# Kernel tuning notes

Hardware: AMD Instinct MI355X
Metric: run time of the kernel (lower is better)

The kernel has to match this reference:

```python
import jax, jax.numpy as jnp
import numpy as np

LN_EPS = 1e-5

def sin_emb(coords, dim):
    # coords [..., 3] -> [..., dim]; dim split evenly over 3 axes, sin/cos halves
    per_axis = dim // 3
    half = per_axis // 2
    freqs = jnp.exp(-jnp.log(10000.0) * jnp.arange(half, dtype=coords.dtype) / max(half - 1, 1))
    ang = coords[..., None] * freqs  # [..., 3, half]
    emb = jnp.concatenate([jnp.sin(ang), jnp.cos(ang)], axis=-1)  # [..., 3, per_axis]
    return emb.reshape(coords.shape[:-1] + (dim,))

def layernorm(x, g, b):
    mu = jnp.mean(x, axis=-1, keepdims=True)
    var = jnp.mean((x - mu) ** 2, axis=-1, keepdims=True)
    return (x - mu) * jax.lax.rsqrt(var + LN_EPS) * g + b

def point_mlp(x, w, b, g, be, act):
    h = layernorm(x @ w + b, g, be)
    return jax.nn.gelu(h, approximate=False) if act else h

def query_ball_point(radius, nsample, xyz):
    # xyz [B,N,3] -> idx [B,N,nsample] (pad with first in-ball index, PointNet++ style)
    N = xyz.shape[1]
    sq = jnp.sum((xyz[:, :, None, :] - xyz[:, None, :, :]) ** 2, axis=-1)  # [B,N,N]
    idx0 = jnp.where(sq > radius * radius, N, jnp.arange(N)[None, None, :])
    idx = jnp.sort(idx0, axis=-1)[:, :, :nsample]
    return jnp.where(idx == N, idx[:, :, :1], idx)

def index_points(points, idx):
    # points [B,N,C], idx [B,S,K] -> [B,S,K,C]
    return jax.vmap(lambda p, i: p[i])(points, idx)

def setup_inputs() -> dict:
    key = jax.random.key(0)
    ks = jax.random.split(key, 20)
    B, N, C_stem, C_tok = 4, 4096, 64, 256
    C_in = C_stem + 3 + 24 + 96  # 187
    w = lambda k, i, o: jax.random.normal(k, (i, o), jnp.float32) * 0.02
    inp = {
        'xyz': jax.random.uniform(ks[0], (B, N, 3), jnp.float32),
        'point_feature': jax.random.normal(ks[1], (B, N, C_stem), jnp.float32),
        # scene_point_mlp
        'w1': w(ks[2], C_in, C_tok), 'b1': jnp.zeros((C_tok,)), 'g1': jnp.ones((C_tok,)), 'be1': jnp.zeros((C_tok,)),
        'w2': w(ks[3], C_tok, C_tok), 'b2': jnp.zeros((C_tok,)), 'g2': jnp.ones((C_tok,)), 'be2': jnp.zeros((C_tok,)),
        # scene_projection
        'pw1': w(ks[4], C_tok, C_tok), 'pb1': jnp.zeros((C_tok,)), 'pg1': jnp.ones((C_tok,)), 'pbe1': jnp.zeros((C_tok,)),
        'pw2': w(ks[5], C_tok, C_tok), 'pb2': jnp.zeros((C_tok,)), 'pg2': jnp.ones((C_tok,)), 'pbe2': jnp.zeros((C_tok,)),
    }
    return inp

def reference(xyz, point_feature, w1, b1, g1, be1, w2, b2, g2, be2,
              pw1, pb1, pg1, pbe1, pw2, pb2, pg2, pbe2):
    radius, K = 0.16, 32
    idx = query_ball_point(radius, K, xyz)                     # [B,N,K]
    grouped_xyz = index_points(xyz, idx)                       # [B,N,K,3]
    grouped_feature = index_points(point_feature, idx)         # [B,N,K,Cs]
    relative_xyz = grouped_xyz - xyz[:, :, None, :]            # [B,N,K,3]
    relative_position = sin_emb(relative_xyz, 24)              # [B,N,K,24]
    absolute_position = sin_emb(xyz, 96)                       # [B,N,96]
    B, N = xyz.shape[0], xyz.shape[1]
    absolute_position = jnp.broadcast_to(absolute_position[:, :, None, :], (B, N, K, 96))
    grouped_input = jnp.concatenate(
        (grouped_feature, relative_xyz, relative_position, absolute_position), axis=-1)
    h = point_mlp(grouped_input, w1, b1, g1, be1, True)
    h = point_mlp(h, w2, b2, g2, be2, False)
    scene_point_feature = jnp.max(h, axis=2)                   # [B,N,C]
    pooled = jnp.max(scene_point_feature, axis=1, keepdims=True)  # [B,1,C]
    t = point_mlp(pooled, pw1, pb1, pg1, pbe1, True)
    global_scene_token = point_mlp(t, pw2, pb2, pg2, pbe2, False)
    return global_scene_token
```

## Files before the change

kernel.cpp:

```cpp
#include <hip/hip_runtime.h>
#include <hip/hip_bf16.h>
#include <math.h>


#define LN_EPS 1e-5f

typedef __attribute__((ext_vector_type(8))) short bf16x8;
typedef __attribute__((ext_vector_type(4))) float f32x4;
typedef __attribute__((ext_vector_type(2))) unsigned int u32x2;
typedef __attribute__((ext_vector_type(4))) unsigned int u32x4;

#if __has_builtin(__builtin_amdgcn_rcpf)
#define FRCP(x) __builtin_amdgcn_rcpf(x)
#else
#define FRCP(x) (1.0f / (x))
#endif

__device__ __forceinline__ unsigned short f2bf(float f) {
    unsigned int x = __float_as_uint(f);
    return (unsigned short)((x + 0x7FFFu + ((x >> 16) & 1u)) >> 16);
}
__device__ __forceinline__ unsigned int pack2(float a, float b) {
    union { __hip_bfloat162 h; unsigned int u; } cvt;
    cvt.h = __float22bfloat162_rn(make_float2(a, b));
    return cvt.u;
}
__device__ __forceinline__ unsigned int fenc(float f) {
    unsigned int u = __float_as_uint(f);
    return (u & 0x80000000u) ? ~u : (u | 0x80000000u);
}
__device__ __forceinline__ float fdec(unsigned int u) {
    return __uint_as_float((u & 0x80000000u) ? (u & 0x7FFFFFFFu) : ~u);
}
__device__ __forceinline__ float gelu_fast(float x) {
    float x2 = x * x;
    float u = x * fmaf(0.0356774081f, x2, 0.7978845608f);
    float e = exp2f(u * -2.8853900818f);
    float r = FRCP(e + 1.0f);
    return x * r;
}
template<int CTRL>
__device__ __forceinline__ float dppadd(float s) {
    int v = __builtin_amdgcn_update_dpp(0, __float_as_int(s), CTRL, 0xF, 0xF, true);
    return s + __int_as_float(v);
}
__device__ __forceinline__ float rowsum16(float x) {
    x = dppadd<0x128>(x);
    x = dppadd<0x124>(x);
    x = dppadd<0x122>(x);
    x = dppadd<0x121>(x);
    return x;
}

__global__ __launch_bounds__(256) void k_prep(
    const float* __restrict__ w1, const float* __restrict__ w2,
    unsigned short* __restrict__ w2T, unsigned short* __restrict__ w1T,
    unsigned int* __restrict__ pooled, int* __restrict__ done)
{
    int t = threadIdx.x, blk = blockIdx.x;
    if (blk < 16) {
        __shared__ unsigned short tile[64][65];
        int tr = blk >> 2, tc = blk & 3;
        #pragma unroll
        for (int rr = 0; rr < 16; ++rr) {
            int kl = rr * 4 + (t >> 6), nl = t & 63;
            tile[kl][nl] = f2bf(w2[(size_t)(tr * 64 + kl) * 256 + tc * 64 + nl]);
        }
        __syncthreads();
        #pragma unroll
        for (int rr = 0; rr < 16; ++rr) {
            int nl = rr * 4 + (t >> 6), kp = t & 63;
            int kl = (kp & 3) * 16 + (kp >> 2);
            w2T[(size_t)(tc * 64 + nl) * 256 + tr * 64 + kp] = tile[kl][nl];
        }
    } else if (blk < 28) {
        __shared__ unsigned short tile[64][65];
        int idx = blk - 16;
        int tr = idx >> 2, tc = idx & 3;
        #pragma unroll
        for (int rr = 0; rr < 16; ++rr) {
            int kl = rr * 4 + (t >> 6), nl = t & 63;
            int kp = tr * 64 + kl;
            float v = 0.f;
            if (kp < 91)                       v = w1[(size_t)kp * 256 + tc * 64 + nl];
            else if (kp >= 92 && kp <= 187)    v = w1[(size_t)(kp - 1) * 256 + tc * 64 + nl];
            tile[kl][nl] = f2bf(v);
        }
        __syncthreads();
        #pragma unroll
        for (int rr = 0; rr < 16; ++rr) {
            int nl = rr * 4 + (t >> 6), kl = t & 63;
            w1T[(size_t)(tc * 64 + nl) * 192 + tr * 64 + kl] = tile[kl][nl];
        }
    } else {
        unsigned int idv = fenc(-1e19f);
        for (int q = t; q < 1024; q += 256) pooled[q] = idv;
        if (t == 0) *done = 0;
    }
}

__global__ __launch_bounds__(512, 4) void k_main(
    const float* __restrict__ xyz, const float* __restrict__ pf,
    const unsigned short* __restrict__ w1T, const unsigned short* __restrict__ w2T,
    const float* __restrict__ b1, const float* __restrict__ g1,
    const float* __restrict__ be1,
    const float* __restrict__ b2, const float* __restrict__ g2,
    const float* __restrict__ be2,
    unsigned int* __restrict__ pooled, int* __restrict__ done,
    const float* __restrict__ pw1, const float* __restrict__ pb1,
    const float* __restrict__ pg1, const float* __restrict__ pbe1,
    const float* __restrict__ pw2, const float* __restrict__ pb2,
    const float* __restrict__ pg2, const float* __restrict__ pbe2,
    float* __restrict__ out)
{
    __shared__ __align__(16) unsigned short smem[128 * 264];
    __shared__ __align__(16) unsigned int epack[4 * 48];
    __shared__ unsigned long long bmask[4][64];
    __shared__ int   idxs[128];
    __shared__ float ctr[4][3];
    __shared__ int   lastf;
    unsigned short* a1s = smem;
    unsigned short* h1s = smem;

    const int N = 4096;
    int tid = threadIdx.x, wv = tid >> 6, lane = tid & 63;
    int lo16 = lane & 15, quad = lane >> 4;
    int wvM = wv >> 2, wvN = wv & 3;
    int b = blockIdx.x & 3;
    int i0 = (blockIdx.x >> 2) * 4;
    size_t base = (size_t)b * N;
    const float* xb = xyz + base * 3;

    bf16x8 bfr0[4];
    #pragma unroll
    for (int nt = 0; nt < 4; ++nt) {
        int n = wvN * 64 + nt * 16 + lo16;
        bfr0[nt] = *(const bf16x8*)&w1T[n * 192 + 0 * 32 + quad * 8];
    }

    if (tid < 12) { int p = tid / 3, a = tid - 3 * p; ctr[p][a] = xb[(i0 + p) * 3 + a]; }
    if (tid < 192) {
        int p = tid / 48, pr = tid - 48 * p;
        float vals[2];
        #pragma unroll
        for (int q = 0; q < 2; ++q) {
            int cc = pr * 2 + q;
            int a = cc >> 5, wI = cc & 31;
            int jf = (wI < 16) ? wI : (wI - 16);
            float coord = xb[(i0 + p) * 3 + a];
            float fr = __expf(-0.61402269146507894f * (float)jf);
            float ang = coord * fr;
            vals[q] = (wI < 16) ? __sinf(ang) : __cosf(ang);
        }
        epack[p * 48 + pr] = pack2(vals[0], vals[1]);
    }
    const double r2d = 0.16 * 0.16;
    float T = (float)r2d;
    if ((double)T > r2d) T = __uint_as_float(__float_as_uint(T) - 1u);
    {
        f32x4 cA = *(const f32x4*)(xb + (size_t)i0 * 3);
        f32x4 cB = *(const f32x4*)(xb + (size_t)i0 * 3 + 4);
        f32x4 cC = *(const f32x4*)(xb + (size_t)i0 * 3 + 8);
        float cx0 = cA.x, cy0 = cA.y, cz0 = cA.z;
        float cx1 = cA.w, cy1 = cB.x, cz1 = cB.y;
        float cx2 = cB.z, cy2 = cB.w, cz2 = cC.x;
        float cx3 = cC.y, cy3 = cC.z, cz3 = cC.w;
        #pragma unroll 2
        for (int i = 0; i < 8; ++i) {
            int chunk = wv * 8 + i;
            int j = chunk * 64 + lane;
            const float* pp = xb + (size_t)j * 3;
            float px = pp[0], py = pp[1], pz = pp[2];
            float dx0 = __fsub_rn(px, cx0), dy0 = __fsub_rn(py, cy0), dz0 = __fsub_rn(pz, cz0);
            float sq0 = __fadd_rn(__fadd_rn(__fmul_rn(dx0, dx0), __fmul_rn(dy0, dy0)),
                                  __fmul_rn(dz0, dz0));
            unsigned long long m0 = __ballot(sq0 <= T);
            float dx1 = __fsub_rn(px, cx1), dy1 = __fsub_rn(py, cy1), dz1 = __fsub_rn(pz, cz1);
            float sq1 = __fadd_rn(__fadd_rn(__fmul_rn(dx1, dx1), __fmul_rn(dy1, dy1)),
                                  __fmul_rn(dz1, dz1));
            unsigned long long m1 = __ballot(sq1 <= T);
            float dx2 = __fsub_rn(px, cx2), dy2 = __fsub_rn(py, cy2), dz2 = __fsub_rn(pz, cz2);
            float sq2 = __fadd_rn(__fadd_rn(__fmul_rn(dx2, dx2), __fmul_rn(dy2, dy2)),
                                  __fmul_rn(dz2, dz2));
            unsigned long long m2 = __ballot(sq2 <= T);
            float dx3 = __fsub_rn(px, cx3), dy3 = __fsub_rn(py, cy3), dz3 = __fsub_rn(pz, cz3);
            float sq3 = __fadd_rn(__fadd_rn(__fmul_rn(dx3, dx3), __fmul_rn(dy3, dy3)),
                                  __fmul_rn(dz3, dz3));
            unsigned long long m3 = __ballot(sq3 <= T);
            if (lane == 0) {
                bmask[0][chunk] = m0; bmask[1][chunk] = m1;
                bmask[2][chunk] = m2; bmask[3][chunk] = m3;
            }
        }
    }
    __syncthreads();
    if (wv < 4) {
        int p = wv;
        unsigned long long m = bmask[p][lane];
        int c = __popcll(m);
        int inc = c;
        #pragma unroll
        for (int d = 1; d <= 32; d <<= 1) {
            int v = __shfl_up(inc, d);
            if (lane >= d) inc += v;
        }
        int exc = inc - c;
        int total = __shfl(inc, 63);
        unsigned long long lm = __ballot(m != 0ull);
        int fl = __ffsll(lm) - 1;
        unsigned long long mf = (unsigned long long)__shfl((long long)m, fl);
        int firstj = fl * 64 + __ffsll(mf) - 1;
        unsigned long long mm = m;
        int t = 0;
        while (mm != 0ull && (exc + t) < 32) {
            int bpos = __ffsll(mm) - 1;
            idxs[p * 32 + exc + t] = lane * 64 + bpos;
            mm &= mm - 1; ++t;
        }
        if (lane >= total && lane < 32) idxs[p * 32 + lane] = firstj;
    }
    __syncthreads();

    {
        int r = tid >> 2, seg = tid & 3;
        int j = idxs[r];
        const f32x4* src = (const f32x4*)(pf + (base + (size_t)j) * 64 + seg * 16);
        f32x4 v0 = src[0], v1 = src[1], v2 = src[2], v3 = src[3];
        u32x4 o0, o1;
        o0.x = pack2(v0.x, v0.y); o0.y = pack2(v0.z, v0.w);
        o0.z = pack2(v1.x, v1.y); o0.w = pack2(v1.z, v1.w);
        o1.x = pack2(v2.x, v2.y); o1.y = pack2(v2.z, v2.w);
        o1.z = pack2(v3.x, v3.y); o1.w = pack2(v3.z, v3.w);
        u32x4* dst = (u32x4*)&a1s[r * 200 + seg * 16];
        dst[0] = o0; dst[1] = o1;
    }
    {
        int r = tid & 127, part = tid >> 7;
        int p = r >> 5;
        int j = idxs[r];
        float rx = xb[j * 3]     - ctr[p][0];
        float ry = xb[j * 3 + 1] - ctr[p][1];
        float rz = xb[j * 3 + 2] - ctr[p][2];
        unsigned short* arow = &a1s[r * 200];
        if (part == 0) {
            *(unsigned int*)&arow[64] = pack2(rx, ry);
            arow[66] = f2bf(rz);
            arow[91] = 0;
            *(u32x2*)&arow[188] = (u32x2){0u, 0u};
        } else {
            int a = part - 1;
            float cv = (a == 0) ? rx : ((a == 1) ? ry : rz);
            const float fr4[4] = {1.f, 0.046415888336127774f,
                                  0.0021544346900318843f, 1e-4f};
            float sn[4], cs[4];
            #pragma unroll
            for (int tt = 0; tt < 4; ++tt) {
                float ang = cv * fr4[tt];
                sn[tt] = __sinf(ang); cs[tt] = __cosf(ang);
            }
            arow[67 + a * 8 + 0] = f2bf(sn[0]); arow[67 + a * 8 + 1] = f2bf(sn[1]);
            arow[67 + a * 8 + 2] = f2bf(sn[2]); arow[67 + a * 8 + 3] = f2bf(sn[3]);
            arow[67 + a * 8 + 4] = f2bf(cs[0]); arow[67 + a * 8 + 5] = f2bf(cs[1]);
            arow[67 + a * 8 + 6] = f2bf(cs[2]); arow[67 + a * 8 + 7] = f2bf(cs[3]);
        }
    }
    {
        int r = tid >> 2, part = tid & 3, p = r >> 5;
        const u32x2* e = (const u32x2*)(epack + p * 48 + part * 12);
        u32x2* dst = (u32x2*)&a1s[r * 200 + 92 + part * 24];
        #pragma unroll
        for (int q = 0; q < 6; ++q) dst[q] = e[q];
    }
    bf16x8 bfr1[4];
    #pragma unroll
    for (int nt = 0; nt < 4; ++nt) {
        int n = wvN * 64 + nt * 16 + lo16;
        bfr1[nt] = *(const bf16x8*)&w1T[n * 192 + 1 * 32 + quad * 8];
    }
    __syncthreads();

    const int arow0 = wvM * 64;
    f32x4 acc[4][4];
    {
        float b1f[4];
        #pragma unroll
        for (int nt = 0; nt < 4; ++nt) b1f[nt] = b1[wvN * 64 + nt * 16 + lo16];
        #pragma unroll
        for (int mt = 0; mt < 4; ++mt)
            #pragma unroll
            for (int nt = 0; nt < 4; ++nt)
                #pragma unroll
                for (int reg = 0; reg < 4; ++reg) acc[mt][nt][reg] = b1f[nt];
    }
    #pragma unroll
    for (int mt = 0; mt < 4; ++mt) {
        bf16x8 afr = *(const bf16x8*)&a1s[(arow0 + mt * 16 + lo16) * 200 + 0 * 32 + quad * 8];
        #pragma unroll
        for (int nt = 0; nt < 4; ++nt)
            acc[mt][nt] = __builtin_amdgcn_mfma_f32_16x16x32_bf16(
                afr, bfr0[nt], acc[mt][nt], 0, 0, 0);
    }
    #pragma unroll
    for (int mt = 0; mt < 4; ++mt) {
        bf16x8 afr = *(const bf16x8*)&a1s[(arow0 + mt * 16 + lo16) * 200 + 1 * 32 + quad * 8];
        #pragma unroll
        for (int nt = 0; nt < 4; ++nt)
            acc[mt][nt] = __builtin_amdgcn_mfma_f32_16x16x32_bf16(
                afr, bfr1[nt], acc[mt][nt], 0, 0, 0);
    }
    for (int ks = 2; ks < 6; ++ks) {
        bf16x8 bfr[4];
        #pragma unroll
        for (int nt = 0; nt < 4; ++nt) {
            int n = wvN * 64 + nt * 16 + lo16;
            bfr[nt] = *(const bf16x8*)&w1T[n * 192 + ks * 32 + quad * 8];
        }
        #pragma unroll
        for (int mt = 0; mt < 4; ++mt) {
            bf16x8 afr = *(const bf16x8*)&a1s[(arow0 + mt * 16 + lo16) * 200 + ks * 32 + quad * 8];
            #pragma unroll
            for (int nt = 0; nt < 4; ++nt)
                acc[mt][nt] = __builtin_amdgcn_mfma_f32_16x16x32_bf16(
                    afr, bfr[nt], acc[mt][nt], 0, 0, 0);
        }
    }

    __shared__ float reds[128][4][2];
    __shared__ float musig[128][2];
    #pragma unroll
    for (int mt = 0; mt < 4; ++mt) {
        #pragma unroll
        for (int reg = 0; reg < 4; ++reg) {
            float s1 = 0.f, s2 = 0.f;
            #pragma unroll
            for (int nt = 0; nt < 4; ++nt) { float v = acc[mt][nt][reg]; s1 += v; s2 = fmaf(v, v, s2); }
            s1 = rowsum16(s1); s2 = rowsum16(s2);
            if (lo16 == 0) {
                int r = arow0 + mt * 16 + quad * 4 + reg;
                reds[r][wvN][0] = s1; reds[r][wvN][1] = s2;
            }
        }
    }
    __syncthreads();
    if (tid < 128) {
        int r = tid;
        float s1 = reds[r][0][0] + reds[r][1][0] + reds[r][2][0] + reds[r][3][0];
        float s2 = reds[r][0][1] + reds[r][1][1] + reds[r][2][1] + reds[r][3][1];
        float mu = s1 * (1.f / 256.f);
        float var = fmaxf(s2 * (1.f / 256.f) - mu * mu, 0.f);
        musig[r][0] = mu; musig[r][1] = rsqrtf(var + LN_EPS);
    }
    __syncthreads();
    {
        float g1f[4], be1f[4];
        #pragma unroll
        for (int nt = 0; nt < 4; ++nt) {
            int n = wvN * 64 + nt * 16 + lo16;
            g1f[nt] = g1[n]; be1f[nt] = be1[n];
        }
        #pragma unroll
        for (int mt = 0; mt < 4; ++mt) {
            #pragma unroll
            for (int reg = 0; reg < 4; ++reg) {
                int r = arow0 + mt * 16 + quad * 4 + reg;
                float mu = musig[r][0], rs = musig[r][1];
                float v0 = gelu_fast(fmaf((acc[mt][0][reg] - mu) * rs, g1f[0], be1f[0]));
                float v1 = gelu_fast(fmaf((acc[mt][1][reg] - mu) * rs, g1f[1], be1f[1]));
                float v2 = gelu_fast(fmaf((acc[mt][2][reg] - mu) * rs, g1f[2], be1f[2]));
                float v3 = gelu_fast(fmaf((acc[mt][3][reg] - mu) * rs, g1f[3], be1f[3]));
                u32x2 w; w.x = pack2(v0, v1); w.y = pack2(v2, v3);
                *(u32x2*)&h1s[r * 264 + wvN * 64 + lo16 * 4] = w;
            }
        }
    }
    __syncthreads();

    {
        float b2f[4];
        #pragma unroll
        for (int nt = 0; nt < 4; ++nt) b2f[nt] = b2[wvN * 64 + nt * 16 + lo16];
        #pragma unroll
        for (int mt = 0; mt < 4; ++mt)
            #pragma unroll
            for (int nt = 0; nt < 4; ++nt)
                #pragma unroll
                for (int reg = 0; reg < 4; ++reg) acc[mt][nt][reg] = b2f[nt];
    }
    for (int ks = 0; ks < 8; ++ks) {
        bf16x8 bfr[4], afr[4];
        #pragma unroll
        for (int nt = 0; nt < 4; ++nt) {
            int n = wvN * 64 + nt * 16 + lo16;
            bfr[nt] = *(const bf16x8*)&w2T[n * 256 + ks * 32 + quad * 8];
        }
        #pragma unroll
        for (int mt = 0; mt < 4; ++mt)
            afr[mt] = *(const bf16x8*)&h1s[(arow0 + mt * 16 + lo16) * 264 + ks * 32 + quad * 8];
        #pragma unroll
        for (int mt = 0; mt < 4; ++mt)
            #pragma unroll
            for (int nt = 0; nt < 4; ++nt)
                acc[mt][nt] = __builtin_amdgcn_mfma_f32_16x16x32_bf16(
                    afr[mt], bfr[nt], acc[mt][nt], 0, 0, 0);
    }

    {
        #pragma unroll
        for (int mt = 0; mt < 4; ++mt) {
            #pragma unroll
            for (int reg = 0; reg < 4; ++reg) {
                float s1 = 0.f, s2 = 0.f;
                #pragma unroll
                for (int nt = 0; nt < 4; ++nt) { float v = acc[mt][nt][reg]; s1 += v; s2 = fmaf(v, v, s2); }
                s1 = rowsum16(s1); s2 = rowsum16(s2);
                if (lo16 == 0) {
                    int r = arow0 + mt * 16 + quad * 4 + reg;
                    reds[r][wvN][0] = s1; reds[r][wvN][1] = s2;
                }
            }
        }
        __syncthreads();
        if (tid < 128) {
            int r = tid;
            float s1 = reds[r][0][0] + reds[r][1][0] + reds[r][2][0] + reds[r][3][0];
            float s2 = reds[r][0][1] + reds[r][1][1] + reds[r][2][1] + reds[r][3][1];
            float mu = s1 * (1.f / 256.f);
            float var = fmaxf(s2 * (1.f / 256.f) - mu * mu, 0.f);
            musig[r][0] = mu; musig[r][1] = rsqrtf(var + LN_EPS);
        }
        __syncthreads();

        float g2f[4], be2f[4];
        #pragma unroll
        for (int nt = 0; nt < 4; ++nt) {
            int n = wvN * 64 + nt * 16 + lo16;
            g2f[nt] = g2[n]; be2f[nt] = be2[n];
        }
        float mx[4] = {-1e30f, -1e30f, -1e30f, -1e30f};
        #pragma unroll
        for (int mt = 0; mt < 4; ++mt) {
            #pragma unroll
            for (int reg = 0; reg < 4; ++reg) {
                int r = arow0 + mt * 16 + quad * 4 + reg;
                float mu = musig[r][0], rs = musig[r][1];
                #pragma unroll
                for (int nt = 0; nt < 4; ++nt) {
                    float v = fmaf((acc[mt][nt][reg] - mu) * rs, g2f[nt], be2f[nt]);
                    mx[nt] = fmaxf(mx[nt], v);
                }
            }
        }
        #pragma unroll
        for (int nt = 0; nt < 4; ++nt) {
            mx[nt] = fmaxf(mx[nt], __shfl_xor(mx[nt], 16));
            mx[nt] = fmaxf(mx[nt], __shfl_xor(mx[nt], 32));
        }
        if (quad == 0) {
            #pragma unroll
            for (int nt = 0; nt < 4; ++nt)
                atomicMax(pooled + b * 256 + wvN * 64 + nt * 16 + lo16, fenc(mx[nt]));
        }
    }

    __syncthreads();
    if (tid == 0) lastf = (atomicAdd(done, 1) == 4095);
    __syncthreads();
    if (!lastf) return;
    if (wv < 4) {
        int bb = wv;
        float* xw = (float*)smem + wv * 512;
        #pragma unroll
        for (int q = 0; q < 4; ++q)
            xw[q * 64 + lane] =
                fdec(atomicMax(&pooled[bb * 256 + q * 64 + lane], 0u));

        float a1[4];
        #pragma unroll
        for (int q = 0; q < 4; ++q) a1[q] = pb1[q * 64 + lane];
        #pragma unroll 4
        for (int k = 0; k < 256; ++k) {
            float xv = xw[k];
            const float* wr = pw1 + (size_t)k * 256 + lane;
            #pragma unroll
            for (int q = 0; q < 4; ++q) a1[q] = fmaf(xv, wr[q * 64], a1[q]);
        }
        float s1 = a1[0] + a1[1] + a1[2] + a1[3];
        float s2 = fmaf(a1[0], a1[0], fmaf(a1[1], a1[1],
                   fmaf(a1[2], a1[2], a1[3] * a1[3])));
        s1 = rowsum16(s1); s2 = rowsum16(s2);
        s1 += __shfl_xor(s1, 16); s2 += __shfl_xor(s2, 16);
        s1 += __shfl_xor(s1, 32); s2 += __shfl_xor(s2, 32);
        float mu = s1 * (1.f / 256.f);
        float rs = rsqrtf(fmaxf(s2 * (1.f / 256.f) - mu * mu, 0.f) + LN_EPS);
        #pragma unroll
        for (int q = 0; q < 4; ++q) {
            int c = q * 64 + lane;
            xw[256 + c] = gelu_fast(fmaf((a1[q] - mu) * rs, pg1[c], pbe1[c]));
        }

        float a2[4];
        #pragma unroll
        for (int q = 0; q < 4; ++q) a2[q] = pb2[q * 64 + lane];
        #pragma unroll 4
        for (int k = 0; k < 256; ++k) {
            float xv = xw[256 + k];
            const float* wr = pw2 + (size_t)k * 256 + lane;
            #pragma unroll
            for (int q = 0; q < 4; ++q) a2[q] = fmaf(xv, wr[q * 64], a2[q]);
        }
        s1 = a2[0] + a2[1] + a2[2] + a2[3];
        s2 = fmaf(a2[0], a2[0], fmaf(a2[1], a2[1],
             fmaf(a2[2], a2[2], a2[3] * a2[3])));
        s1 = rowsum16(s1); s2 = rowsum16(s2);
        s1 += __shfl_xor(s1, 16); s2 += __shfl_xor(s2, 16);
        s1 += __shfl_xor(s1, 32); s2 += __shfl_xor(s2, 32);
        mu = s1 * (1.f / 256.f);
        rs = rsqrtf(fmaxf(s2 * (1.f / 256.f) - mu * mu, 0.f) + LN_EPS);
        #pragma unroll
        for (int q = 0; q < 4; ++q) {
            int c = q * 64 + lane;
            out[bb * 256 + c] = fmaf((a2[q] - mu) * rs, pg2[c], pbe2[c]);
        }
    }
}

extern "C" void kernel_launch(void* const* d_in, const int* in_sizes, int n_in,
                              void* d_out, int out_size, void* d_ws, size_t ws_size,
                              hipStream_t stream)
{
    char* ws = (char*)d_ws;
    unsigned short* w2T    = (unsigned short*)ws;
    unsigned short* w1T    = (unsigned short*)(ws + (128u << 10));
    unsigned int*   pooled = (unsigned int*)(ws + (224u << 10));
    int*            done   = (int*)(ws + (228u << 10));

    k_prep<<<29, 256, 0, stream>>>((const float*)d_in[2], (const float*)d_in[6],
                                   w2T, w1T, pooled, done);
    k_main<<<4096, 512, 0, stream>>>((const float*)d_in[0], (const float*)d_in[1],
                                     w1T, w2T,
                                     (const float*)d_in[3], (const float*)d_in[4],
                                     (const float*)d_in[5],
                                     (const float*)d_in[7], (const float*)d_in[8],
                                     (const float*)d_in[9], pooled, done,
                                     (const float*)d_in[10], (const float*)d_in[11],
                                     (const float*)d_in[12], (const float*)d_in[13],
                                     (const float*)d_in[14], (const float*)d_in[15],
                                     (const float*)d_in[16], (const float*)d_in[17],
                                     (float*)d_out);
}
```

Baseline: 444.0 us.

## Give each wave a private 16-row slab across all 256 output columns

Reorganizes both MLP GEMMs so each of the 8 waves owns 16 rows and computes all 256 output columns, rather than splitting a 128x256 tile 2x4 across waves. LayerNorm statistics are then reduced within a wave, which removes the shared-memory reduction arrays and several block-wide barriers. Per-block max pooling first goes through shared-memory atomics before a single global atomicMax per channel. The w2T permutation in k_prep is changed to match the new access pattern. Weights are now read from global/L2 on every k-step with no register prefetch, and each wave holds 16 accumulators, which may raise register pressure and weight traffic.

Result: slower. 1.006 ms (+126.5%).

```diff
diff --git a/kernel.cpp b/kernel.cpp
--- a/kernel.cpp
+++ b/kernel.cpp
@@ -69,9 +69,10 @@
         __syncthreads();
         #pragma unroll
         for (int rr = 0; rr < 16; ++rr) {
-            int nl = rr * 4 + (t >> 6), kp = t & 63;
-            int kl = (kp & 3) * 16 + (kp >> 2);
-            w2T[(size_t)(tc * 64 + nl) * 256 + tr * 64 + kp] = tile[kl][nl];
+            int nl = rr * 4 + (t >> 6), kl = t & 63;
+            int ch = tr * 64 + kl;
+            int kp = ((ch & 15) << 4) | (ch >> 4);
+            w2T[(size_t)(tc * 64 + nl) * 256 + kp] = tile[kl][nl];
         }
     } else if (blk < 28) {
         __shared__ unsigned short tile[64][65];
@@ -113,31 +114,25 @@
     const float* __restrict__ pg2, const float* __restrict__ pbe2,
     float* __restrict__ out)
 {
-    __shared__ __align__(16) unsigned short smem[128 * 264];
+    __shared__ __align__(16) unsigned short smem[8 * 4224];
     __shared__ __align__(16) unsigned int epack[4 * 48];
     __shared__ unsigned long long bmask[4][64];
     __shared__ int   idxs[128];
     __shared__ float ctr[4][3];
+    __shared__ unsigned int pool_s[256];
     __shared__ int   lastf;
-    unsigned short* a1s = smem;
-    unsigned short* h1s = smem;
 
     const int N = 4096;
     int tid = threadIdx.x, wv = tid >> 6, lane = tid & 63;
     int lo16 = lane & 15, quad = lane >> 4;
-    int wvM = wv >> 2, wvN = wv & 3;
     int b = blockIdx.x & 3;
     int i0 = (blockIdx.x >> 2) * 4;
     size_t base = (size_t)b * N;
     const float* xb = xyz + base * 3;
 
-    bf16x8 bfr0[4];
-    #pragma unroll
-    for (int nt = 0; nt < 4; ++nt) {
-        int n = wvN * 64 + nt * 16 + lo16;
-        bfr0[nt] = *(const bf16x8*)&w1T[n * 192 + 0 * 32 + quad * 8];
-    }
-
+    #define AROW(r) (smem + (((r) >> 4) * 4224) + (((r) & 15) * 200))
+
+    if (tid < 256) pool_s[tid] = fenc(-1e19f);
     if (tid < 12) { int p = tid / 3, a = tid - 3 * p; ctr[p][a] = xb[(i0 + p) * 3 + a]; }
     if (tid < 192) {
         int p = tid / 48, pr = tid - 48 * p;
@@ -231,7 +226,7 @@
         o0.z = pack2(v1.x, v1.y); o0.w = pack2(v1.z, v1.w);
         o1.x = pack2(v2.x, v2.y); o1.y = pack2(v2.z, v2.w);
         o1.z = pack2(v3.x, v3.y); o1.w = pack2(v3.z, v3.w);
-        u32x4* dst = (u32x4*)&a1s[r * 200 + seg * 16];
+        u32x4* dst = (u32x4*)(AROW(r) + seg * 16);
         dst[0] = o0; dst[1] = o1;
     }
     {
@@ -241,7 +236,7 @@
         float rx = xb[j * 3]     - ctr[p][0];
         float ry = xb[j * 3 + 1] - ctr[p][1];
         float rz = xb[j * 3 + 2] - ctr[p][2];
-        unsigned short* arow = &a1s[r * 200];
+        unsigned short* arow = AROW(r);
         if (part == 0) {
             *(unsigned int*)&arow[64] = pack2(rx, ry);
             arow[66] = f2bf(rz);
@@ -267,201 +262,101 @@
     {
         int r = tid >> 2, part = tid & 3, p = r >> 5;
         const u32x2* e = (const u32x2*)(epack + p * 48 + part * 12);
-        u32x2* dst = (u32x2*)&a1s[r * 200 + 92 + part * 24];
+        u32x2* dst = (u32x2*)(AROW(r) + 92 + part * 24);
         #pragma unroll
         for (int q = 0; q < 6; ++q) dst[q] = e[q];
     }
-    bf16x8 bfr1[4];
-    #pragma unroll
-    for (int nt = 0; nt < 4; ++nt) {
-        int n = wvN * 64 + nt * 16 + lo16;
-        bfr1[nt] = *(const bf16x8*)&w1T[n * 192 + 1 * 32 + quad * 8];
-    }
-    __syncthreads();
-
-    const int arow0 = wvM * 64;
-    f32x4 acc[4][4];
-    {
-        float b1f[4];
-        #pragma unroll
-        for (int nt = 0; nt < 4; ++nt) b1f[nt] = b1[wvN * 64 + nt * 16 + lo16];
-        #pragma unroll
-        for (int mt = 0; mt < 4; ++mt)
-            #pragma unroll
-            for (int nt = 0; nt < 4; ++nt)
-                #pragma unroll
-                for (int reg = 0; reg < 4; ++reg) acc[mt][nt][reg] = b1f[nt];
-    }
-    #pragma unroll
-    for (int mt = 0; mt < 4; ++mt) {
-        bf16x8 afr = *(const bf16x8*)&a1s[(arow0 + mt * 16 + lo16) * 200 + 0 * 32 + quad * 8];
-        #pragma unroll
-        for (int nt = 0; nt < 4; ++nt)
-            acc[mt][nt] = __builtin_amdgcn_mfma_f32_16x16x32_bf16(
-                afr, bfr0[nt], acc[mt][nt], 0, 0, 0);
-    }
-    #pragma unroll
-    for (int mt = 0; mt < 4; ++mt) {
-        bf16x8 afr = *(const bf16x8*)&a1s[(arow0 + mt * 16 + lo16) * 200 + 1 * 32 + quad * 8];
-        #pragma unroll
-        for (int nt = 0; nt < 4; ++nt)
-            acc[mt][nt] = __builtin_amdgcn_mfma_f32_16x16x32_bf16(
-                afr, bfr1[nt], acc[mt][nt], 0, 0, 0);
-    }
-    for (int ks = 2; ks < 6; ++ks) {
-        bf16x8 bfr[4];
-        #pragma unroll
-        for (int nt = 0; nt < 4; ++nt) {
-            int n = wvN * 64 + nt * 16 + lo16;
-            bfr[nt] = *(const bf16x8*)&w1T[n * 192 + ks * 32 + quad * 8];
-        }
-        #pragma unroll
-        for (int mt = 0; mt < 4; ++mt) {
-            bf16x8 afr = *(const bf16x8*)&a1s[(arow0 + mt * 16 + lo16) * 200 + ks * 32 + quad * 8];
-            #pragma unroll
-            for (int nt = 0; nt < 4; ++nt)
-                acc[mt][nt] = __builtin_amdgcn_mfma_f32_16x16x32_bf16(
-                    afr, bfr[nt], acc[mt][nt], 0, 0, 0);
-        }
-    }
-
-    __shared__ float reds[128][4][2];
-    __shared__ float musig[128][2];
-    #pragma unroll
-    for (int mt = 0; mt < 4; ++mt) {
-        #pragma unroll
-        for (int reg = 0; reg < 4; ++reg) {
-            float s1 = 0.f, s2 = 0.f;
-            #pragma unroll
-            for (int nt = 0; nt < 4; ++nt) { float v = acc[mt][nt][reg]; s1 += v; s2 = fmaf(v, v, s2); }
-            s1 = rowsum16(s1); s2 = rowsum16(s2);
-            if (lo16 == 0) {
-                int r = arow0 + mt * 16 + quad * 4 + reg;
-                reds[r][wvN][0] = s1; reds[r][wvN][1] = s2;
-            }
-        }
-    }
-    __syncthreads();
-    if (tid < 128) {
-        int r = tid;
-        float s1 = reds[r][0][0] + reds[r][1][0] + reds[r][2][0] + reds[r][3][0];
-        float s2 = reds[r][0][1] + reds[r][1][1] + reds[r][2][1] + reds[r][3][1];
+    __syncthreads();
+
+    unsigned short* slab = smem + wv * 4224;
+
+    f32x4 acc[16];
+    #pragma unroll
+    for (int nt = 0; nt < 16; ++nt) {
+        float bv = b1[nt * 16 + lo16];
+        acc[nt] = (f32x4){bv, bv, bv, bv};
+    }
+    #pragma unroll
+    for (int ks = 0; ks < 6; ++ks) {
+        bf16x8 afr = *(const bf16x8*)&slab[lo16 * 200 + ks * 32 + quad * 8];
+        #pragma unroll
+        for (int nt = 0; nt < 16; ++nt) {
+            bf16x8 bfr = *(const bf16x8*)&w1T[(nt * 16 + lo16) * 192 + ks * 32 + quad * 8];
+            acc[nt] = __builtin_amdgcn_mfma_f32_16x16x32_bf16(afr, bfr, acc[nt], 0, 0, 0);
+        }
+    }
+
+    float muA[4], rsA[4];
+    #pragma unroll
+    for (int reg = 0; reg < 4; ++reg) {
+        float s1 = 0.f, s2 = 0.f;
+        #pragma unroll
+        for (int nt = 0; nt < 16; ++nt) { float v = acc[nt][reg]; s1 += v; s2 = fmaf(v, v, s2); }
+        s1 = rowsum16(s1); s2 = rowsum16(s2);
         float mu = s1 * (1.f / 256.f);
         float var = fmaxf(s2 * (1.f / 256.f) - mu * mu, 0.f);
-        musig[r][0] = mu; musig[r][1] = rsqrtf(var + LN_EPS);
-    }
-    __syncthreads();
-    {
-        float g1f[4], be1f[4];
-        #pragma unroll
-        for (int nt = 0; nt < 4; ++nt) {
-            int n = wvN * 64 + nt * 16 + lo16;
-            g1f[nt] = g1[n]; be1f[nt] = be1[n];
-        }
-        #pragma unroll
-        for (int mt = 0; mt < 4; ++mt) {
-            #pragma unroll
-            for (int reg = 0; reg < 4; ++reg) {
-                int r = arow0 + mt * 16 + quad * 4 + reg;
-                float mu = musig[r][0], rs = musig[r][1];
-                float v0 = gelu_fast(fmaf((acc[mt][0][reg] - mu) * rs, g1f[0], be1f[0]));
-                float v1 = gelu_fast(fmaf((acc[mt][1][reg] - mu) * rs, g1f[1], be1f[1]));
-                float v2 = gelu_fast(fmaf((acc[mt][2][reg] - mu) * rs, g1f[2], be1f[2]));
-                float v3 = gelu_fast(fmaf((acc[mt][3][reg] - mu) * rs, g1f[3], be1f[3]));
-                u32x2 w; w.x = pack2(v0, v1); w.y = pack2(v2, v3);
-                *(u32x2*)&h1s[r * 264 + wvN * 64 + lo16 * 4] = w;
-            }
-        }
-    }
-    __syncthreads();
-
-    {
-        float b2f[4];
-        #pragma unroll
-        for (int nt = 0; nt < 4; ++nt) b2f[nt] = b2[wvN * 64 + nt * 16 + lo16];
-        #pragma unroll
-        for (int mt = 0; mt < 4; ++mt)
-            #pragma unroll
-            for (int nt = 0; nt < 4; ++nt)
-                #pragma unroll
-                for (int reg = 0; reg < 4; ++reg) acc[mt][nt][reg] = b2f[nt];
-    }
+        muA[reg] = mu; rsA[reg] = rsqrtf(var + LN_EPS);
+    }
+    #pragma unroll
+    for (int reg = 0; reg < 4; ++reg) {
+        int lr = quad * 4 + reg;
+        float mu = muA[reg], rs = rsA[reg];
+        #pragma unroll
+        for (int g4 = 0; g4 < 4; ++g4) {
+            float v0 = gelu_fast(fmaf((acc[g4 * 4 + 0][reg] - mu) * rs,
+                                      g1[(g4 * 4 + 0) * 16 + lo16], be1[(g4 * 4 + 0) * 16 + lo16]));
+            float v1 = gelu_fast(fmaf((acc[g4 * 4 + 1][reg] - mu) * rs,
+                                      g1[(g4 * 4 + 1) * 16 + lo16], be1[(g4 * 4 + 1) * 16 + lo16]));
+            float v2 = gelu_fast(fmaf((acc[g4 * 4 + 2][reg] - mu) * rs,
+                                      g1[(g4 * 4 + 2) * 16 + lo16], be1[(g4 * 4 + 2) * 16 + lo16]));
+            float v3 = gelu_fast(fmaf((acc[g4 * 4 + 3][reg] - mu) * rs,
+                                      g1[(g4 * 4 + 3) * 16 + lo16], be1[(g4 * 4 + 3) * 16 + lo16]));
+            u32x2 wp; wp.x = pack2(v0, v1); wp.y = pack2(v2, v3);
+            *(u32x2*)&slab[lr * 264 + lo16 * 16 + g4 * 4] = wp;
+        }
+    }
+
+    #pragma unroll
+    for (int nt = 0; nt < 16; ++nt) {
+        float bv = b2[nt * 16 + lo16];
+        acc[nt] = (f32x4){bv, bv, bv, bv};
+    }
+    #pragma unroll
     for (int ks = 0; ks < 8; ++ks) {
-        bf16x8 bfr[4], afr[4];
-        #pragma unroll
-        for (int nt = 0; nt < 4; ++nt) {
-            int n = wvN * 64 + nt * 16 + lo16;
-            bfr[nt] = *(const bf16x8*)&w2T[n * 256 + ks * 32 + quad * 8];
-        }
-        #pragma unroll
-        for (int mt = 0; mt < 4; ++mt)
-            afr[mt] = *(const bf16x8*)&h1s[(arow0 + mt * 16 + lo16) * 264 + ks * 32 + quad * 8];
-        #pragma unroll
-        for (int mt = 0; mt < 4; ++mt)
-            #pragma unroll
-            for (int nt = 0; nt < 4; ++nt)
-                acc[mt][nt] = __builtin_amdgcn_mfma_f32_16x16x32_bf16(
-                    afr[mt], bfr[nt], acc[mt][nt], 0, 0, 0);
-    }
-
-    {
-        #pragma unroll
-        for (int mt = 0; mt < 4; ++mt) {
-            #pragma unroll
-            for (int reg = 0; reg < 4; ++reg) {
-                float s1 = 0.f, s2 = 0.f;
-                #pragma unroll
-                for (int nt = 0; nt < 4; ++nt) { float v = acc[mt][nt][reg]; s1 += v; s2 = fmaf(v, v, s2); }
-                s1 = rowsum16(s1); s2 = rowsum16(s2);
-                if (lo16 == 0) {
-                    int r = arow0 + mt * 16 + quad * 4 + reg;
-                    reds[r][wvN][0] = s1; reds[r][wvN][1] = s2;
-                }
-            }
-        }
-        __syncthreads();
-        if (tid < 128) {
-            int r = tid;
-            float s1 = reds[r][0][0] + reds[r][1][0] + reds[r][2][0] + reds[r][3][0];
-            float s2 = reds[r][0][1] + reds[r][1][1] + reds[r][2][1] + reds[r][3][1];
-            float mu = s1 * (1.f / 256.f);
-            float var = fmaxf(s2 * (1.f / 256.f) - mu * mu, 0.f);
-            musig[r][0] = mu; musig[r][1] = rsqrtf(var + LN_EPS);
-        }
-        __syncthreads();
-
-        float g2f[4], be2f[4];
-        #pragma unroll
-        for (int nt = 0; nt < 4; ++nt) {
-            int n = wvN * 64 + nt * 16 + lo16;
-            g2f[nt] = g2[n]; be2f[nt] = be2[n];
-        }
-        float mx[4] = {-1e30f, -1e30f, -1e30f, -1e30f};
-        #pragma unroll
-        for (int mt = 0; mt < 4; ++mt) {
-            #pragma unroll
-            for (int reg = 0; reg < 4; ++reg) {
-                int r = arow0 + mt * 16 + quad * 4 + reg;
-                float mu = musig[r][0], rs = musig[r][1];
-                #pragma unroll
-                for (int nt = 0; nt < 4; ++nt) {
-                    float v = fmaf((acc[mt][nt][reg] - mu) * rs, g2f[nt], be2f[nt]);
-                    mx[nt] = fmaxf(mx[nt], v);
-                }
-            }
-        }
-        #pragma unroll
-        for (int nt = 0; nt < 4; ++nt) {
-            mx[nt] = fmaxf(mx[nt], __shfl_xor(mx[nt], 16));
-            mx[nt] = fmaxf(mx[nt], __shfl_xor(mx[nt], 32));
-        }
-        if (quad == 0) {
-            #pragma unroll
-            for (int nt = 0; nt < 4; ++nt)
-                atomicMax(pooled + b * 256 + wvN * 64 + nt * 16 + lo16, fenc(mx[nt]));
-        }
-    }
-
+        bf16x8 afr = *(const bf16x8*)&slab[lo16 * 264 + ks * 32 + quad * 8];
+        #pragma unroll
+        for (int nt = 0; nt < 16; ++nt) {
+            bf16x8 bfr = *(const bf16x8*)&w2T[(nt * 16 + lo16) * 256 + ks * 32 + quad * 8];
+            acc[nt] = __builtin_amdgcn_mfma_f32_16x16x32_bf16(afr, bfr, acc[nt], 0, 0, 0);
+        }
+    }
+
+    #pragma unroll
+    for (int reg = 0; reg < 4; ++reg) {
+        float s1 = 0.f, s2 = 0.f;
+        #pragma unroll
+        for (int nt = 0; nt < 16; ++nt) { float v = acc[nt][reg]; s1 += v; s2 = fmaf(v, v, s2); }
+        s1 = rowsum16(s1); s2 = rowsum16(s2);
+        float mu = s1 * (1.f / 256.f);
+        float var = fmaxf(s2 * (1.f / 256.f) - mu * mu, 0.f);
+        muA[reg] = mu; rsA[reg] = rsqrtf(var + LN_EPS);
+    }
+    #pragma unroll
+    for (int nt = 0; nt < 16; ++nt) {
+        float g = g2[nt * 16 + lo16], be = be2[nt * 16 + lo16];
+        float m = -1e30f;
+        #pragma unroll
+        for (int reg = 0; reg < 4; ++reg) {
+            float v = fmaf((acc[nt][reg] - muA[reg]) * rsA[reg], g, be);
+            m = fmaxf(m, v);
+        }
+        m = fmaxf(m, __shfl_xor(m, 16));
+        m = fmaxf(m, __shfl_xor(m, 32));
+        if (quad == 0) atomicMax(&pool_s[nt * 16 + lo16], fenc(m));
+    }
+
+    __syncthreads();
+    if (tid < 256) atomicMax(pooled + b * 256 + tid, pool_s[tid]);
     __syncthreads();
     if (tid == 0) lastf = (atomicAdd(done, 1) == 4095);
     __syncthreads();
@@ -522,6 +417,7 @@
             out[bb * 256 + c] = fmaf((a2[q] - mu) * rs, pg2[c], pbe2[c]);
         }
     }
+    #undef AROW
 }
 
 extern "C" void kernel_launch(void* const* d_in, const int* in_sizes, int n_in,
```

## Precompute per-point first-layer projections to shrink grouped GEMM K dimension

Applied to the files above, without the earlier changes.

The first MLP layer is split by linearity. The point-feature part (64 inputs) is projected once per point into U, and the absolute-position part plus bias (96 inputs) once per center into V, both in a new pre-pass kernel. The main kernel then gathers U rows by neighbor index, adds V, and runs only a K=32 MFMA over the relative xyz and relative sin embedding. This cuts the per-group layer-1 GEMM from K=192 to K=32, and the gathered features are no longer converted to bf16 in the main kernel. In exchange it adds an extra launch, 32 MB of fp32 U/V workspace traffic, and fp32 gathers of 1 KB rows per neighbor instead of 256 B bf16 feature rows.

After: 407.2 us. 1.09x faster.

```diff
diff --git a/kernel.cpp b/kernel.cpp
--- a/kernel.cpp
+++ b/kernel.cpp
@@ -54,7 +54,8 @@
 
 __global__ __launch_bounds__(256) void k_prep(
     const float* __restrict__ w1, const float* __restrict__ w2,
-    unsigned short* __restrict__ w2T, unsigned short* __restrict__ w1T,
+    unsigned short* __restrict__ w2T, unsigned short* __restrict__ w1aT,
+    unsigned short* __restrict__ w1cT, unsigned short* __restrict__ w1bT,
     unsigned int* __restrict__ pooled, int* __restrict__ done)
 {
     int t = threadIdx.x, blk = blockIdx.x;
@@ -73,24 +74,47 @@
             int kl = (kp & 3) * 16 + (kp >> 2);
             w2T[(size_t)(tc * 64 + nl) * 256 + tr * 64 + kp] = tile[kl][nl];
         }
+    } else if (blk < 20) {
+        __shared__ unsigned short tile[64][65];
+        int tc = blk - 16;
+        #pragma unroll
+        for (int rr = 0; rr < 16; ++rr) {
+            int kl = rr * 4 + (t >> 6), nl = t & 63;
+            tile[kl][nl] = f2bf(w1[(size_t)kl * 256 + tc * 64 + nl]);
+        }
+        __syncthreads();
+        #pragma unroll
+        for (int rr = 0; rr < 16; ++rr) {
+            int nl = rr * 4 + (t >> 6), kl = t & 63;
+            w1aT[(size_t)(tc * 64 + nl) * 64 + kl] = tile[kl][nl];
+        }
     } else if (blk < 28) {
         __shared__ unsigned short tile[64][65];
-        int idx = blk - 16;
-        int tr = idx >> 2, tc = idx & 3;
+        int idx = blk - 20;
+        int tr2 = idx >> 2, tc = idx & 3;
         #pragma unroll
         for (int rr = 0; rr < 16; ++rr) {
             int kl = rr * 4 + (t >> 6), nl = t & 63;
-            int kp = tr * 64 + kl;
+            int k = tr2 * 64 + kl;
             float v = 0.f;
-            if (kp < 91)                       v = w1[(size_t)kp * 256 + tc * 64 + nl];
-            else if (kp >= 92 && kp <= 187)    v = w1[(size_t)(kp - 1) * 256 + tc * 64 + nl];
+            if (k < 96) v = w1[(size_t)(91 + k) * 256 + tc * 64 + nl];
             tile[kl][nl] = f2bf(v);
         }
         __syncthreads();
         #pragma unroll
         for (int rr = 0; rr < 16; ++rr) {
             int nl = rr * 4 + (t >> 6), kl = t & 63;
-            w1T[(size_t)(tc * 64 + nl) * 192 + tr * 64 + kl] = tile[kl][nl];
+            int k = tr2 * 64 + kl;
+            if (k < 96)
+                w1cT[(size_t)(tc * 64 + nl) * 96 + k] = tile[kl][nl];
+        }
+    } else if (blk == 28) {
+        int n = t;
+        #pragma unroll
+        for (int k = 0; k < 32; ++k) {
+            unsigned short v = 0;
+            if (k < 27) v = f2bf(w1[(size_t)(64 + k) * 256 + n]);
+            w1bT[(size_t)n * 32 + k] = v;
         }
     } else {
         unsigned int idv = fenc(-1e19f);
@@ -99,11 +123,126 @@
     }
 }
 
+__global__ __launch_bounds__(256) void k_pre(
+    const float* __restrict__ xyz, const float* __restrict__ pf,
+    const unsigned short* __restrict__ w1aT, const unsigned short* __restrict__ w1cT,
+    const float* __restrict__ b1,
+    float* __restrict__ U_p, float* __restrict__ V_p)
+{
+    __shared__ __align__(16) unsigned short ptile[64 * 72];
+    __shared__ __align__(16) unsigned short etile[64 * 104];
+    int tid = threadIdx.x, wv = tid >> 6, lane = tid & 63;
+    int lo16 = lane & 15, quad = lane >> 4;
+    int rows0 = blockIdx.x * 64;
+
+    {
+        int r = tid >> 2, seg = tid & 3;
+        const f32x4* src = (const f32x4*)(pf + (size_t)(rows0 + r) * 64 + seg * 16);
+        f32x4 v0 = src[0], v1 = src[1], v2 = src[2], v3 = src[3];
+        u32x4 o0, o1;
+        o0.x = pack2(v0.x, v0.y); o0.y = pack2(v0.z, v0.w);
+        o0.z = pack2(v1.x, v1.y); o0.w = pack2(v1.z, v1.w);
+        o1.x = pack2(v2.x, v2.y); o1.y = pack2(v2.z, v2.w);
+        o1.z = pack2(v3.x, v3.y); o1.w = pack2(v3.z, v3.w);
+        u32x4* dst = (u32x4*)&ptile[r * 72 + seg * 16];
+        dst[0] = o0; dst[1] = o1;
+    }
+    {
+        int r = tid & 63, grp = tid >> 6;
+        float c0 = xyz[(size_t)(rows0 + r) * 3];
+        float c1 = xyz[(size_t)(rows0 + r) * 3 + 1];
+        float c2 = xyz[(size_t)(rows0 + r) * 3 + 2];
+        #pragma unroll
+        for (int q = 0; q < 12; ++q) {
+            int pr = grp * 12 + q;
+            float vals[2];
+            #pragma unroll
+            for (int qq = 0; qq < 2; ++qq) {
+                int cc = pr * 2 + qq;
+                int a = cc >> 5, wI = cc & 31;
+                int jf = (wI < 16) ? wI : (wI - 16);
+                float coord = (a == 0) ? c0 : ((a == 1) ? c1 : c2);
+                float fr = __expf(-0.61402269146507894f * (float)jf);
+                float ang = coord * fr;
+                vals[qq] = (wI < 16) ? __sinf(ang) : __cosf(ang);
+            }
+            *(unsigned int*)&etile[r * 104 + 2 * pr] = pack2(vals[0], vals[1]);
+        }
+    }
+    __syncthreads();
+
+    f32x4 acc[4][4];
+    #pragma unroll
+    for (int mt = 0; mt < 4; ++mt)
+        #pragma unroll
+        for (int nt = 0; nt < 4; ++nt) acc[mt][nt] = (f32x4){0.f, 0.f, 0.f, 0.f};
+    #pragma unroll
+    for (int ks = 0; ks < 2; ++ks) {
+        bf16x8 bfr[4];
+        #pragma unroll
+        for (int nt = 0; nt < 4; ++nt) {
+            int n = wv * 64 + nt * 16 + lo16;
+            bfr[nt] = *(const bf16x8*)&w1aT[(size_t)n * 64 + ks * 32 + quad * 8];
+        }
+        #pragma unroll
+        for (int mt = 0; mt < 4; ++mt) {
+            bf16x8 afr = *(const bf16x8*)&ptile[(mt * 16 + lo16) * 72 + ks * 32 + quad * 8];
+            #pragma unroll
+            for (int nt = 0; nt < 4; ++nt)
+                acc[mt][nt] = __builtin_amdgcn_mfma_f32_16x16x32_bf16(
+                    afr, bfr[nt], acc[mt][nt], 0, 0, 0);
+        }
+    }
+    #pragma unroll
+    for (int mt = 0; mt < 4; ++mt)
+        #pragma unroll
+        for (int reg = 0; reg < 4; ++reg) {
+            f32x4 o = {acc[mt][0][reg], acc[mt][1][reg], acc[mt][2][reg], acc[mt][3][reg]};
+            *(f32x4*)&U_p[(size_t)(rows0 + mt * 16 + quad * 4 + reg) * 256 + wv * 64 + lo16 * 4] = o;
+        }
+
+    {
+        float b1f[4];
+        #pragma unroll
+        for (int nt = 0; nt < 4; ++nt) b1f[nt] = b1[wv * 64 + nt * 16 + lo16];
+        #pragma unroll
+        for (int mt = 0; mt < 4; ++mt)
+            #pragma unroll
+            for (int nt = 0; nt < 4; ++nt)
+                #pragma unroll
+                for (int reg = 0; reg < 4; ++reg) acc[mt][nt][reg] = b1f[nt];
+    }
+    #pragma unroll
+    for (int ks = 0; ks < 3; ++ks) {
+        bf16x8 bfr[4];
+        #pragma unroll
+        for (int nt = 0; nt < 4; ++nt) {
+            int n = wv * 64 + nt * 16 + lo16;
+            bfr[nt] = *(const bf16x8*)&w1cT[(size_t)n * 96 + ks * 32 + quad * 8];
+        }
+        #pragma unroll
+        for (int mt = 0; mt < 4; ++mt) {
+            bf16x8 afr = *(const bf16x8*)&etile[(mt * 16 + lo16) * 104 + ks * 32 + quad * 8];
+            #pragma unroll
+            for (int nt = 0; nt < 4; ++nt)
+                acc[mt][nt] = __builtin_amdgcn_mfma_f32_16x16x32_bf16(
+                    afr, bfr[nt], acc[mt][nt], 0, 0, 0);
+        }
+    }
+    #pragma unroll
+    for (int mt = 0; mt < 4; ++mt)
+        #pragma unroll
+        for (int reg = 0; reg < 4; ++reg) {
+            f32x4 o = {acc[mt][0][reg], acc[mt][1][reg], acc[mt][2][reg], acc[mt][3][reg]};
+            *(f32x4*)&V_p[(size_t)(rows0 + mt * 16 + quad * 4 + reg) * 256 + wv * 64 + lo16 * 4] = o;
+        }
+}
+
 __global__ __launch_bounds__(512, 4) void k_main(
-    const float* __restrict__ xyz, const float* __restrict__ pf,
-    const unsigned short* __restrict__ w1T, const unsigned short* __restrict__ w2T,
-    const float* __restrict__ b1, const float* __restrict__ g1,
-    const float* __restrict__ be1,
+    const float* __restrict__ xyz,
+    const unsigned short* __restrict__ w1bT, const unsigned short* __restrict__ w2T,
+    const float* __restrict__ U_p, const float* __restrict__ V_p,
+    const float* __restrict__ g1, const float* __restrict__ be1,
     const float* __restrict__ b2, const float* __restrict__ g2,
     const float* __restrict__ be2,
     unsigned int* __restrict__ pooled, int* __restrict__ done,
@@ -114,13 +253,14 @@
     float* __restrict__ out)
 {
     __shared__ __align__(16) unsigned short smem[128 * 264];
-    __shared__ __align__(16) unsigned int epack[4 * 48];
     __shared__ unsigned long long bmask[4][64];
     __shared__ int   idxs[128];
     __shared__ float ctr[4][3];
+    __shared__ float reds[128][4][2];
+    __shared__ float musig[128][2];
     __shared__ int   lastf;
-    unsigned short* a1s = smem;
-    unsigned short* h1s = smem;
+    unsigned short* rels = smem;
+    unsigned short* h1s  = smem;
 
     const int N = 4096;
     int tid = threadIdx.x, wv = tid >> 6, lane = tid & 63;
@@ -131,29 +271,14 @@
     size_t base = (size_t)b * N;
     const float* xb = xyz + base * 3;
 
-    bf16x8 bfr0[4];
+    bf16x8 bfrR[4];
     #pragma unroll
     for (int nt = 0; nt < 4; ++nt) {
         int n = wvN * 64 + nt * 16 + lo16;
-        bfr0[nt] = *(const bf16x8*)&w1T[n * 192 + 0 * 32 + quad * 8];
+        bfrR[nt] = *(const bf16x8*)&w1bT[(size_t)n * 32 + quad * 8];
     }
 
     if (tid < 12) { int p = tid / 3, a = tid - 3 * p; ctr[p][a] = xb[(i0 + p) * 3 + a]; }
-    if (tid < 192) {
-        int p = tid / 48, pr = tid - 48 * p;
-        float vals[2];
-        #pragma unroll
-        for (int q = 0; q < 2; ++q) {
-            int cc = pr * 2 + q;
-            int a = cc >> 5, wI = cc & 31;
-            int jf = (wI < 16) ? wI : (wI - 16);
-            float coord = xb[(i0 + p) * 3 + a];
-            float fr = __expf(-0.61402269146507894f * (float)jf);
-            float ang = coord * fr;
-            vals[q] = (wI < 16) ? __sinf(ang) : __cosf(ang);
-        }
-        epack[p * 48 + pr] = pack2(vals[0], vals[1]);
-    }
     const double r2d = 0.16 * 0.16;
     float T = (float)r2d;
     if ((double)T > r2d) T = __uint_as_float(__float_as_uint(T) - 1u);
@@ -222,31 +347,18 @@
     __syncthreads();
 
     {
-        int r = tid >> 2, seg = tid & 3;
-        int j = idxs[r];
-        const f32x4* src = (const f32x4*)(pf + (base + (size_t)j) * 64 + seg * 16);
-        f32x4 v0 = src[0], v1 = src[1], v2 = src[2], v3 = src[3];
-        u32x4 o0, o1;
-        o0.x = pack2(v0.x, v0.y); o0.y = pack2(v0.z, v0.w);
-        o0.z = pack2(v1.x, v1.y); o0.w = pack2(v1.z, v1.w);
-        o1.x = pack2(v2.x, v2.y); o1.y = pack2(v2.z, v2.w);
-        o1.z = pack2(v3.x, v3.y); o1.w = pack2(v3.z, v3.w);
-        u32x4* dst = (u32x4*)&a1s[r * 200 + seg * 16];
-        dst[0] = o0; dst[1] = o1;
-    }
-    {
         int r = tid & 127, part = tid >> 7;
         int p = r >> 5;
         int j = idxs[r];
         float rx = xb[j * 3]     - ctr[p][0];
         float ry = xb[j * 3 + 1] - ctr[p][1];
         float rz = xb[j * 3 + 2] - ctr[p][2];
-        unsigned short* arow = &a1s[r * 200];
+        unsigned short* arow = &rels[r * 40];
         if (part == 0) {
-            *(unsigned int*)&arow[64] = pack2(rx, ry);
-            arow[66] = f2bf(rz);
-            arow[91] = 0;
-            *(u32x2*)&arow[188] = (u32x2){0u, 0u};
+            *(unsigned int*)&arow[0] = pack2(rx, ry);
+            arow[2] = f2bf(rz);
+            arow[27] = 0;
+            *(u32x2*)&arow[28] = (u32x2){0u, 0u};
         } else {
             int a = part - 1;
             float cv = (a == 0) ? rx : ((a == 1) ? ry : rz);
@@ -258,75 +370,38 @@
                 float ang = cv * fr4[tt];
                 sn[tt] = __sinf(ang); cs[tt] = __cosf(ang);
             }
-            arow[67 + a * 8 + 0] = f2bf(sn[0]); arow[67 + a * 8 + 1] = f2bf(sn[1]);
-            arow[67 + a * 8 + 2] = f2bf(sn[2]); arow[67 + a * 8 + 3] = f2bf(sn[3]);
-            arow[67 + a * 8 + 4] = f2bf(cs[0]); arow[67 + a * 8 + 5] = f2bf(cs[1]);
-            arow[67 + a * 8 + 6] = f2bf(cs[2]); arow[67 + a * 8 + 7] = f2bf(cs[3]);
-        }
-    }
-    {
-        int r = tid >> 2, part = tid & 3, p = r >> 5;
-        const u32x2* e = (const u32x2*)(epack + p * 48 + part * 12);
-        u32x2* dst = (u32x2*)&a1s[r * 200 + 92 + part * 24];
-        #pragma unroll
-        for (int q = 0; q < 6; ++q) dst[q] = e[q];
-    }
-    bf16x8 bfr1[4];
-    #pragma unroll
-    for (int nt = 0; nt < 4; ++nt) {
-        int n = wvN * 64 + nt * 16 + lo16;
-        bfr1[nt] = *(const bf16x8*)&w1T[n * 192 + 1 * 32 + quad * 8];
+            arow[3 + a * 8 + 0] = f2bf(sn[0]); arow[3 + a * 8 + 1] = f2bf(sn[1]);
+            arow[3 + a * 8 + 2] = f2bf(sn[2]); arow[3 + a * 8 + 3] = f2bf(sn[3]);
+            arow[3 + a * 8 + 4] = f2bf(cs[0]); arow[3 + a * 8 + 5] = f2bf(cs[1]);
+            arow[3 + a * 8 + 6] = f2bf(cs[2]); arow[3 + a * 8 + 7] = f2bf(cs[3]);
+        }
     }
     __syncthreads();
 
     const int arow0 = wvM * 64;
     f32x4 acc[4][4];
-    {
-        float b1f[4];
-        #pragma unroll
-        for (int nt = 0; nt < 4; ++nt) b1f[nt] = b1[wvN * 64 + nt * 16 + lo16];
-        #pragma unroll
-        for (int mt = 0; mt < 4; ++mt)
-            #pragma unroll
-            for (int nt = 0; nt < 4; ++nt)
-                #pragma unroll
-                for (int reg = 0; reg < 4; ++reg) acc[mt][nt][reg] = b1f[nt];
-    }
     #pragma unroll
     for (int mt = 0; mt < 4; ++mt) {
-        bf16x8 afr = *(const bf16x8*)&a1s[(arow0 + mt * 16 + lo16) * 200 + 0 * 32 + quad * 8];
+        int cl = wvM * 2 + (mt >> 1);
+        f32x4 vv = *(const f32x4*)&V_p[(size_t)(base + i0 + cl) * 256 + wvN * 64 + lo16 * 4];
+        #pragma unroll
+        for (int reg = 0; reg < 4; ++reg) {
+            int r = arow0 + mt * 16 + quad * 4 + reg;
+            int j = idxs[r];
+            f32x4 uu = *(const f32x4*)&U_p[(size_t)(base + j) * 256 + wvN * 64 + lo16 * 4];
+            #pragma unroll
+            for (int nt = 0; nt < 4; ++nt) acc[mt][nt][reg] = uu[nt] + vv[nt];
+        }
+    }
+    #pragma unroll
+    for (int mt = 0; mt < 4; ++mt) {
+        bf16x8 afr = *(const bf16x8*)&rels[(arow0 + mt * 16 + lo16) * 40 + quad * 8];
         #pragma unroll
         for (int nt = 0; nt < 4; ++nt)
             acc[mt][nt] = __builtin_amdgcn_mfma_f32_16x16x32_bf16(
-                afr, bfr0[nt], acc[mt][nt], 0, 0, 0);
-    }
-    #pragma unroll
-    for (int mt = 0; mt < 4; ++mt) {
-        bf16x8 afr = *(const bf16x8*)&a1s[(arow0 + mt * 16 + lo16) * 200 + 1 * 32 + quad * 8];
-        #pragma unroll
-        for (int nt = 0; nt < 4; ++nt)
-            acc[mt][nt] = __builtin_amdgcn_mfma_f32_16x16x32_bf16(
-                afr, bfr1[nt], acc[mt][nt], 0, 0, 0);
-    }
-    for (int ks = 2; ks < 6; ++ks) {
-        bf16x8 bfr[4];
-        #pragma unroll
-        for (int nt = 0; nt < 4; ++nt) {
-            int n = wvN * 64 + nt * 16 + lo16;
-            bfr[nt] = *(const bf16x8*)&w1T[n * 192 + ks * 32 + quad * 8];
-        }
-        #pragma unroll
-        for (int mt = 0; mt < 4; ++mt) {
-            bf16x8 afr = *(const bf16x8*)&a1s[(arow0 + mt * 16 + lo16) * 200 + ks * 32 + quad * 8];
-            #pragma unroll
-            for (int nt = 0; nt < 4; ++nt)
-                acc[mt][nt] = __builtin_amdgcn_mfma_f32_16x16x32_bf16(
-                    afr, bfr[nt], acc[mt][nt], 0, 0, 0);
-        }
-    }
-
-    __shared__ float reds[128][4][2];
-    __shared__ float musig[128][2];
+                afr, bfrR[nt], acc[mt][nt], 0, 0, 0);
+    }
+
     #pragma unroll
     for (int mt = 0; mt < 4; ++mt) {
         #pragma unroll
@@ -391,7 +466,7 @@
         #pragma unroll
         for (int nt = 0; nt < 4; ++nt) {
             int n = wvN * 64 + nt * 16 + lo16;
-            bfr[nt] = *(const bf16x8*)&w2T[n * 256 + ks * 32 + quad * 8];
+            bfr[nt] = *(const bf16x8*)&w2T[(size_t)n * 256 + ks * 32 + quad * 8];
         }
         #pragma unroll
         for (int mt = 0; mt < 4; ++mt)
@@ -530,16 +605,24 @@
 {
     char* ws = (char*)d_ws;
     unsigned short* w2T    = (unsigned short*)ws;
-    unsigned short* w1T    = (unsigned short*)(ws + (128u << 10));
+    unsigned short* w1aT   = (unsigned short*)(ws + (128u << 10));
+    unsigned short* w1cT   = (unsigned short*)(ws + (160u << 10));
+    unsigned short* w1bT   = (unsigned short*)(ws + (208u << 10));
     unsigned int*   pooled = (unsigned int*)(ws + (224u << 10));
     int*            done   = (int*)(ws + (228u << 10));
-
-    k_prep<<<29, 256, 0, stream>>>((const float*)d_in[2], (const float*)d_in[6],
-                                   w2T, w1T, pooled, done);
-    k_main<<<4096, 512, 0, stream>>>((const float*)d_in[0], (const float*)d_in[1],
-                                     w1T, w2T,
-                                     (const float*)d_in[3], (const float*)d_in[4],
-                                     (const float*)d_in[5],
+    float*          U_p    = (float*)(ws + (256u << 10));
+    float*          V_p    = (float*)(ws + (256u << 10) + (16u << 20));
+
+    const float* xyz = (const float*)d_in[0];
+    const float* pf  = (const float*)d_in[1];
+    const float* w1  = (const float*)d_in[2];
+    const float* b1  = (const float*)d_in[3];
+
+    k_prep<<<30, 256, 0, stream>>>(w1, (const float*)d_in[6],
+                                   w2T, w1aT, w1cT, w1bT, pooled, done);
+    k_pre<<<256, 256, 0, stream>>>(xyz, pf, w1aT, w1cT, b1, U_p, V_p);
+    k_main<<<4096, 512, 0, stream>>>(xyz, w1bT, w2T, U_p, V_p,
+                                     (const float*)d_in[4], (const float*)d_in[5],
                                      (const float*)d_in[7], (const float*)d_in[8],
                                      (const float*)d_in[9], pooled, done,
                                      (const float*)d_in[10], (const float*)d_in[11],
```
